# Performance work log

Hardware: AMD Instinct MI355X
Metric: run time of the kernel (lower is better)

Reference implementation:

```python
import jax, jax.numpy as jnp
import numpy as np

BN_EPS = 1e-5


def conv1x1(x, w, b):
    # x: [B,C,H,W], w: [O,C], b: [O] -> [B,O,H,W]
    return jnp.einsum('bchw,oc->bohw', x, w) + b[None, :, None, None]


def setup_inputs() -> dict:
    key = jax.random.key(0)
    ks = jax.random.split(key, 11)
    B, C, H, W = 8, 1024, 64, 32
    hid = 64  # C * rd_ratio (1/16)
    s = 0.02
    return {
        'x': jax.random.normal(ks[0], (B, C, H, W), dtype=jnp.float32),
        'theta_w': jax.random.normal(ks[1], (hid, C), dtype=jnp.float32) * s,
        'theta_b': jax.random.normal(ks[2], (hid,), dtype=jnp.float32) * s,
        'phi_w': jax.random.normal(ks[3], (hid, C), dtype=jnp.float32) * s,
        'phi_b': jax.random.normal(ks[4], (hid,), dtype=jnp.float32) * s,
        'g_w': jax.random.normal(ks[5], (hid, C), dtype=jnp.float32) * s,
        'g_b': jax.random.normal(ks[6], (hid,), dtype=jnp.float32) * s,
        'w_w': jax.random.normal(ks[7], (C, hid), dtype=jnp.float32) * s,
        'w_b': jax.random.normal(ks[8], (C,), dtype=jnp.float32) * s,
        'bn_gamma': jax.random.normal(ks[9], (C,), dtype=jnp.float32) * 0.1 + 1.0,
        'bn_beta': jax.random.normal(ks[10], (C,), dtype=jnp.float32) * 0.1,
    }


def reference(x, theta_w, theta_b, phi_w, phi_b, g_w, g_b, w_w, w_b, bn_gamma, bn_beta):
    B, C, H, W = x.shape
    hid = theta_w.shape[0]
    N = H * W
    theta = conv1x1(x, theta_w, theta_b).reshape(B, hid, N).transpose(0, 2, 1)  # [B,N,d]
    phi = conv1x1(x, phi_w, phi_b).reshape(B, hid, N)                           # [B,d,N]
    g = conv1x1(x, g_w, g_b).reshape(B, hid, N).transpose(0, 2, 1)              # [B,N,d]
    f = jnp.einsum('bnd,bdm->bnm', theta, phi) / N                              # [B,N,N]
    y = jnp.einsum('bnm,bmd->bnd', f, g)                                        # [B,N,d]
    y = y.transpose(0, 2, 1).reshape(B, hid, H, W)
    wy = conv1x1(y, w_w, w_b)                                                   # [B,C,H,W]
    # BatchNorm2d in training mode: batch statistics over (B,H,W), biased variance
    mean = wy.mean(axis=(0, 2, 3), keepdims=True)
    var = wy.var(axis=(0, 2, 3), keepdims=True)
    norm = (wy - mean) * jax.lax.rsqrt(var + BN_EPS)
    out = norm * bn_gamma[None, :, None, None] + bn_beta[None, :, None, None]
    return out + x
```

## Files before the change

### kernel.cpp

```cpp
#include <hip/hip_runtime.h>

#define B_    8
#define C_    1024
#define HID   64
#define N_    2048
#define RTOT  192

typedef __attribute__((ext_vector_type(8))) short   bf16x8;
typedef __attribute__((ext_vector_type(8))) unsigned short ush8;
typedef __attribute__((ext_vector_type(4))) unsigned short ush4;
typedef __attribute__((ext_vector_type(4))) float   f32x4;

#define WSB_WBF   ((size_t)0)
#define WSB_TPG   ((size_t)393216)
#define WSB_THT   ((size_t)6684672)
#define WSB_M     ((size_t)8781824)
#define WSB_G     ((size_t)8912896)
#define WSB_S     ((size_t)9043968)
#define WSB_WMBF  ((size_t)9046016)
#define WSB_SC    ((size_t)10094592)
#define WSB_SH    ((size_t)10098688)
#define WSB_XT    ((size_t)10102784)
#define WSB_P     WSB_XT
#define PSTRIDE   66048
#define POFF_G    32768
#define POFF_S    65536

static __device__ __forceinline__ unsigned short f2bf(float f) {
    union { float f; unsigned u; } v; v.f = f;
    unsigned r = v.u + 0x7fffu + ((v.u >> 16) & 1u);
    return (unsigned short)(r >> 16);
}
static __device__ __forceinline__ float bf2f(unsigned short h) {
    union { unsigned u; float f; } v; v.u = ((unsigned)h) << 16;
    return v.f;
}

static __device__ __forceinline__ void gload16(const unsigned short* g, unsigned short* l) {
    __builtin_amdgcn_global_load_lds(
        (const __attribute__((address_space(1))) unsigned int*)g,
        (__attribute__((address_space(3))) unsigned int*)l, 16, 0, 0);
}

__global__ __launch_bounds__(256) void wcvt(
    const float* __restrict__ tw, const float* __restrict__ pw,
    const float* __restrict__ gw, unsigned short* __restrict__ wbf)
{
    int idx = blockIdx.x * 256 + threadIdx.x;
    int r = idx >> 10, k = idx & 1023;
    float v = (r < 64) ? tw[(size_t)r * 1024 + k]
            : (r < 128) ? pw[(size_t)(r - 64) * 1024 + k]
                        : gw[(size_t)(r - 128) * 1024 + k];
    wbf[idx] = f2bf(v);
}

__global__ __launch_bounds__(256) void xpose(
    const float* __restrict__ x, unsigned short* __restrict__ xT)
{
    const int n0 = blockIdx.x * 64, c0 = blockIdx.y * 64, b = blockIdx.z;
    const int t = threadIdx.x;
    __shared__ unsigned short tile[64][66];

    const float* xb = x + ((size_t)b * C_ + c0) * N_ + n0;
#pragma unroll
    for (int p = 0; p < 2; p++) {
        const int m  = t & 15;
        const int cp = (t >> 4) + 16 * p;
        const int cl = 2 * cp;
        f32x4 v0 = *(const f32x4*)(xb + (size_t)cl * N_ + m * 4);
        f32x4 v1 = *(const f32x4*)(xb + (size_t)(cl + 1) * N_ + m * 4);
#pragma unroll
        for (int r2 = 0; r2 < 4; r2++) {
            unsigned val = (unsigned)f2bf(v0[r2]) | ((unsigned)f2bf(v1[r2]) << 16);
            *(unsigned*)&tile[m * 4 + r2][cl] = val;
        }
    }
    __syncthreads();
    unsigned short* ob = xT + ((size_t)b * N_ + n0) * C_ + c0;
#pragma unroll
    for (int r = 0; r < 2; r++) {
        const int nl   = (t >> 3) + 32 * r;
        const int c8   = (t & 7) * 8;
        uint4 u;
        u.x = *(unsigned*)&tile[nl][c8];
        u.y = *(unsigned*)&tile[nl][c8 + 2];
        u.z = *(unsigned*)&tile[nl][c8 + 4];
        u.w = *(unsigned*)&tile[nl][c8 + 6];
        *(uint4*)(ob + (size_t)nl * C_ + c8) = u;
    }
}

__global__ __launch_bounds__(256, 4) void proj_mfma(
    const unsigned short* __restrict__ xT, const unsigned short* __restrict__ wbf,
    const float* __restrict__ tb, const float* __restrict__ pb,
    const float* __restrict__ gb, unsigned short* __restrict__ tpgbf,
    unsigned short* __restrict__ thT)
{
    const int b = blockIdx.z, rh = blockIdx.y, n0 = blockIdx.x * 64;
    const int t = threadIdx.x, w = t >> 6, L = t & 63;
    const int wn = w & 1, wc = w >> 1;
    const int lr = L & 15, q = L >> 4;

    __shared__ unsigned short Abuf[2][64][64];
    __shared__ unsigned short Bbuf[2][96][64];

    f32x4 acc[2][3] = {};

    auto stage = [&](int cb, int k0) {
#pragma unroll
        for (int i = 0; i < 2; i++) {
            int o = (i * 256 + t) * 16;
            int row = o >> 7, slot = (o >> 4) & 7, ss = slot ^ (row & 7);
            gload16(xT + ((size_t)b * N_ + n0 + row) * C_ + k0 + ss * 8,
                    &Abuf[cb][0][0] + o / 2);
        }
#pragma unroll
        for (int i = 0; i < 3; i++) {
            int o = (i * 256 + t) * 16;
            int row = o >> 7, slot = (o >> 4) & 7, ss = slot ^ (row & 7);
            gload16(wbf + ((size_t)(96 * rh + row)) * 1024 + k0 + ss * 8,
                    &Bbuf[cb][0][0] + o / 2);
        }
    };

    int cur = 0;
    stage(0, 0);
    asm volatile("s_waitcnt vmcnt(0)" ::: "memory");
    __syncthreads();

    const int swz = lr & 7;
    for (int s = 0; s < 16; s++) {
        if (s < 15) stage(cur ^ 1, (s + 1) * 64);
#pragma unroll
        for (int ksub = 0; ksub < 2; ksub++) {
            bf16x8 Af[2], Bf[3];
#pragma unroll
            for (int fa = 0; fa < 2; fa++)
                Af[fa] = *(const bf16x8*)&Abuf[cur][wn * 32 + fa * 16 + lr]
                                               [((ksub * 4 + q) ^ swz) * 8];
#pragma unroll
            for (int j = 0; j < 3; j++)
                Bf[j] = *(const bf16x8*)&Bbuf[cur][wc * 48 + j * 16 + lr]
                                              [((ksub * 4 + q) ^ swz) * 8];
#pragma unroll
            for (int fa = 0; fa < 2; fa++)
#pragma unroll
                for (int j = 0; j < 3; j++)
                    acc[fa][j] = __builtin_amdgcn_mfma_f32_16x16x32_bf16(
                        Af[fa], Bf[j], acc[fa][j], 0, 0, 0);
        }
        asm volatile("s_waitcnt vmcnt(0)" ::: "memory");
        __syncthreads();
        cur ^= 1;
    }

#pragma unroll
    for (int fa = 0; fa < 2; fa++)
#pragma unroll
        for (int j = 0; j < 3; j++) {
            int rcol = 96 * rh + 48 * wc + 16 * j + lr;
            float bias = (rcol < 64) ? tb[rcol]
                       : (rcol < 128) ? pb[rcol - 64] : gb[rcol - 128];
            ush4 o;
#pragma unroll
            for (int rr = 0; rr < 4; rr++) o[rr] = f2bf(acc[fa][j][rr] + bias);
            int nglob = n0 + wn * 32 + fa * 16 + q * 4;
            *(ush4*)(tpgbf + ((size_t)b * RTOT + rcol) * N_ + nglob) = o;
            if (rcol < HID) {
#pragma unroll
                for (int rr = 0; rr < 4; rr++)
                    thT[((size_t)b * N_ + nglob + rr) * HID + rcol] = o[rr];
            }
        }
}

__global__ __launch_bounds__(256) void gram_mfma(
    const unsigned short* __restrict__ tpgbf, float* __restrict__ P)
{
    const int kc = blockIdx.x, p = blockIdx.y, b = blockIdx.z;
    const int t = threadIdx.x, w = t >> 6, L = t & 63;
    const int lr = L & 15, q = L >> 4;
    const unsigned short* base = tpgbf + (size_t)b * RTOT * N_;
    const unsigned short* Arow = base + (p ? 0 : (size_t)64 * N_);
    const unsigned short* Brow = base + (p ? 0 : (size_t)128 * N_);
    const unsigned short* ap = Arow + ((size_t)(16 * w + lr)) * N_ + kc * 256 + q * 8;
    const unsigned short* bp = Brow + ((size_t)lr) * N_ + kc * 256 + q * 8;

    bf16x8 ones;
#pragma unroll
    for (int j = 0; j < 8; j++) ones[j] = (short)0x3F80;

    f32x4 acc[4] = {};
    f32x4 accs = {};
#pragma unroll
    for (int it = 0; it < 8; ++it) {
        const int kn = it * 32;
        bf16x8 a = *(const bf16x8*)(ap + kn);
#pragma unroll
        for (int g = 0; g < 4; g++) {
            bf16x8 bb = *(const bf16x8*)(bp + (size_t)g * 16 * N_ + kn);
            acc[g] = __builtin_amdgcn_mfma_f32_16x16x32_bf16(a, bb, acc[g], 0, 0, 0);
        }
        if (p) accs = __builtin_amdgcn_mfma_f32_16x16x32_bf16(a, ones, accs, 0, 0, 0);
    }
    float* outp = P + (size_t)kc * PSTRIDE + (p ? POFF_G : 0) + b * (HID * HID);
#pragma unroll
    for (int g = 0; g < 4; g++)
#pragma unroll
        for (int r = 0; r < 4; r++) {
            int row = 16 * w + q * 4 + r, col = 16 * g + lr;
            outp[row * HID + col] = acc[g][r];
        }
    if (p && lr == 0) {
#pragma unroll
        for (int r = 0; r < 4; r++)
            P[(size_t)kc * PSTRIDE + POFF_S + b * HID + 16 * w + q * 4 + r] = accs[r];
    }
}

__global__ __launch_bounds__(256) void reduceMGS(
    const float* __restrict__ P, float* __restrict__ out)
{
    int idx = blockIdx.x * 256 + threadIdx.x;
    float s = 0.f;
#pragma unroll
    for (int kc = 0; kc < 8; kc++) s += P[(size_t)kc * PSTRIDE + idx];
    out[idx] = s;
}

__global__ __launch_bounds__(512) void wmstat(
    const float* __restrict__ ww, const float* __restrict__ Mm,
    const float* __restrict__ S, const float* __restrict__ G,
    const float* __restrict__ wb, const float* __restrict__ gamma,
    const float* __restrict__ beta, unsigned short* __restrict__ wmbf,
    float* __restrict__ scale, float* __restrict__ shift2)
{
    const int c = blockIdx.x;
    const int t = threadIdx.x;
    const int b = t >> 6, lane = t & 63;
    const float wbc = wb[c];
    const float* wr = ww + (size_t)c * HID;

    const float* mr = Mm + ((size_t)b * HID + lane) * HID;
    float acc = 0.f;
#pragma unroll
    for (int d = 0; d < HID; d += 4) {
        float4 m4 = *(const float4*)(mr + d);
        acc += wr[d] * m4.x + wr[d + 1] * m4.y + wr[d + 2] * m4.z + wr[d + 3] * m4.w;
    }
    unsigned short us = f2bf(acc * (1.0f / N_));
    wmbf[((size_t)b * C_ + c) * HID + lane] = us;
    float v = bf2f(us);
    float sv = S[b * HID + lane];
    float t1 = v * sv;
    for (int off = 32; off; off >>= 1) t1 += __shfl_down(t1, off);
    t1 = __shfl(t1, 0);

    const f32x4* Gb4 = (const f32x4*)(G + (size_t)b * HID * HID + (size_t)lane * HID);
    float inner = 0.f;
#pragma unroll
    for (int fo = 0; fo < 16; fo++) {
        f32x4 g4 = Gb4[fo];
        inner = fmaf(g4[0], __shfl(v, 4 * fo + 0), inner);
        inner = fmaf(g4[1], __shfl(v, 4 * fo + 1), inner);
        inner = fmaf(g4[2], __shfl(v, 4 * fo + 2), inner);
        inner = fmaf(g4[3], __shfl(v, 4 * fo + 3), inner);
    }
    float qq = v * inner;
    for (int off = 32; off; off >>= 1) qq += __shfl_down(qq, off);
    qq = __shfl(qq, 0);

    __shared__ float red[16];
    if (lane == 0) {
        red[b] = t1;
        red[8 + b] = qq + 2.f * wbc * t1;
    }
    __syncthreads();
    if (t == 0) {
        float asum = 0.f, asq = 0.f;
#pragma unroll
        for (int i = 0; i < 8; i++) { asum += red[i]; asq += red[8 + i]; }
        const float cnt = (float)B_ * (float)N_;
        const float inv = 1.0f / cnt;
        float mean = (asum + cnt * wbc) * inv;
        float e2   = (asq + cnt * wbc * wbc) * inv;
        float var  = e2 - mean * mean;
        float sc   = gamma[c] * rsqrtf(var + 1e-5f);
        scale[c]  = sc;
        shift2[c] = beta[c] - mean * sc + sc * wbc;
    }
}

__global__ __launch_bounds__(256) void finalk_mfma(
    const unsigned short* __restrict__ wmbf, const unsigned short* __restrict__ thT,
    const float* __restrict__ x, const float* __restrict__ scale,
    const float* __restrict__ shift2, float* __restrict__ out)
{
    const int b = blockIdx.z, c0 = blockIdx.y * 64, n0 = blockIdx.x * 64;
    const int t = threadIdx.x, w = t >> 6, L = t & 63;
    const int lr = L & 15, q = L >> 4;

    const unsigned short* ap = thT + ((size_t)b * N_ + n0 + 16 * w + lr) * HID + q * 8;
    const unsigned short* bp = wmbf + ((size_t)b * C_ + c0 + lr) * HID + q * 8;

    float4 xv[4];
    size_t xoff[4];
#pragma unroll
    for (int g = 0; g < 4; g++) {
        xoff[g] = ((size_t)b * C_ + c0 + 16 * g + lr) * N_ + n0 + 16 * w + q * 4;
        xv[g] = *(const float4*)(x + xoff[g]);
    }

    bf16x8 A0 = *(const bf16x8*)(ap);
    bf16x8 A1 = *(const bf16x8*)(ap + 32);
    f32x4 acc[4] = {};
#pragma unroll
    for (int g = 0; g < 4; g++) {
        bf16x8 Bg0 = *(const bf16x8*)(bp + (size_t)g * 16 * HID);
        bf16x8 Bg1 = *(const bf16x8*)(bp + (size_t)g * 16 * HID + 32);
        acc[g] = __builtin_amdgcn_mfma_f32_16x16x32_bf16(A0, Bg0, acc[g], 0, 0, 0);
        acc[g] = __builtin_amdgcn_mfma_f32_16x16x32_bf16(A1, Bg1, acc[g], 0, 0, 0);
    }
#pragma unroll
    for (int g = 0; g < 4; g++) {
        int c = c0 + 16 * g + lr;
        float sc = scale[c], sh = shift2[c];
        float4 o;
        o.x = fmaf(sc, acc[g][0], sh) + xv[g].x;
        o.y = fmaf(sc, acc[g][1], sh) + xv[g].y;
        o.z = fmaf(sc, acc[g][2], sh) + xv[g].z;
        o.w = fmaf(sc, acc[g][3], sh) + xv[g].w;
        *(float4*)(out + xoff[g]) = o;
    }
}

extern "C" void kernel_launch(void* const* d_in, const int* in_sizes, int n_in,
                              void* d_out, int out_size, void* d_ws, size_t ws_size,
                              hipStream_t stream)
{
    const float* x  = (const float*)d_in[0];
    const float* tw = (const float*)d_in[1];
    const float* tb = (const float*)d_in[2];
    const float* pw = (const float*)d_in[3];
    const float* pb = (const float*)d_in[4];
    const float* gw = (const float*)d_in[5];
    const float* gb = (const float*)d_in[6];
    const float* ww = (const float*)d_in[7];
    const float* wb = (const float*)d_in[8];
    const float* gamma = (const float*)d_in[9];
    const float* beta  = (const float*)d_in[10];
    float* out = (float*)d_out;

    char* ws = (char*)d_ws;
    unsigned short* wbf   = (unsigned short*)(ws + WSB_WBF);
    unsigned short* tpgbf = (unsigned short*)(ws + WSB_TPG);
    unsigned short* thT   = (unsigned short*)(ws + WSB_THT);
    float* Mm   = (float*)(ws + WSB_M);
    float* S    = (float*)(ws + WSB_S);
    float* Gg   = (float*)(ws + WSB_G);
    unsigned short* wmbf = (unsigned short*)(ws + WSB_WMBF);
    float* scl  = (float*)(ws + WSB_SC);
    float* shf  = (float*)(ws + WSB_SH);
    unsigned short* xT = (unsigned short*)(ws + WSB_XT);
    float* P    = (float*)(ws + WSB_P);

    wcvt<<<dim3(RTOT * 1024 / 256), 256, 0, stream>>>(tw, pw, gw, wbf);
    xpose<<<dim3(32, 16, B_), 256, 0, stream>>>(x, xT);
    proj_mfma<<<dim3(32, 2, B_), 256, 0, stream>>>(xT, wbf, tb, pb, gb, tpgbf, thT);
    gram_mfma<<<dim3(8, 2, B_), 256, 0, stream>>>(tpgbf, P);
    reduceMGS<<<dim3(258), 256, 0, stream>>>(P, Mm);
    wmstat<<<C_, 512, 0, stream>>>(ww, Mm, S, Gg, wb, gamma, beta, wmbf, scl, shf);
    finalk_mfma<<<dim3(32, 16, B_), 256, 0, stream>>>(wmbf, thT, x, scl, shf, out);
}
```

Measured before the change: 217.5 us.

## Merge weight cast into transpose kernel and drop split-K gram reduction

Fuses the weight bf16 conversion into the transpose kernel as an extra grid slice, and makes the gram kernel accumulate over the full sequence in one block per (pair,batch), writing M, G and S directly. This removes two kernel launches and the partial-sum buffer round trip. In exchange, the gram stage now runs only 16 blocks with a long serial K loop, which sharply lowers its parallelism.

```diff
diff --git a/kernel.cpp b/kernel.cpp
--- a/kernel.cpp
+++ b/kernel.cpp
@@ -21,10 +21,6 @@
 #define WSB_SC    ((size_t)10094592)
 #define WSB_SH    ((size_t)10098688)
 #define WSB_XT    ((size_t)10102784)
-#define WSB_P     WSB_XT
-#define PSTRIDE   66048
-#define POFF_G    32768
-#define POFF_S    65536
 
 static __device__ __forceinline__ unsigned short f2bf(float f) {
     union { float f; unsigned u; } v; v.f = f;
@@ -42,23 +38,28 @@
         (__attribute__((address_space(3))) unsigned int*)l, 16, 0, 0);
 }
 
-__global__ __launch_bounds__(256) void wcvt(
+__global__ __launch_bounds__(256) void prep(
+    const float* __restrict__ x, unsigned short* __restrict__ xT,
     const float* __restrict__ tw, const float* __restrict__ pw,
     const float* __restrict__ gw, unsigned short* __restrict__ wbf)
 {
-    int idx = blockIdx.x * 256 + threadIdx.x;
-    int r = idx >> 10, k = idx & 1023;
-    float v = (r < 64) ? tw[(size_t)r * 1024 + k]
-            : (r < 128) ? pw[(size_t)(r - 64) * 1024 + k]
-                        : gw[(size_t)(r - 128) * 1024 + k];
-    wbf[idx] = f2bf(v);
-}
-
-__global__ __launch_bounds__(256) void xpose(
-    const float* __restrict__ x, unsigned short* __restrict__ xT)
-{
+    const int t = threadIdx.x;
+    if (blockIdx.z == 8) {
+        const int bid = blockIdx.y * 32 + blockIdx.x;
+#pragma unroll
+        for (int rep = 0; rep < 2; rep++) {
+            int idx = bid * 512 + rep * 256 + t;
+            if (idx < RTOT * 1024) {
+                int r = idx >> 10, k = idx & 1023;
+                float v = (r < 64) ? tw[(size_t)r * 1024 + k]
+                        : (r < 128) ? pw[(size_t)(r - 64) * 1024 + k]
+                                    : gw[(size_t)(r - 128) * 1024 + k];
+                wbf[idx] = f2bf(v);
+            }
+        }
+        return;
+    }
     const int n0 = blockIdx.x * 64, c0 = blockIdx.y * 64, b = blockIdx.z;
-    const int t = threadIdx.x;
     __shared__ unsigned short tile[64][66];
 
     const float* xb = x + ((size_t)b * C_ + c0) * N_ + n0;
@@ -175,16 +176,17 @@
 }
 
 __global__ __launch_bounds__(256) void gram_mfma(
-    const unsigned short* __restrict__ tpgbf, float* __restrict__ P)
-{
-    const int kc = blockIdx.x, p = blockIdx.y, b = blockIdx.z;
+    const unsigned short* __restrict__ tpgbf, float* __restrict__ Mm,
+    float* __restrict__ Gg, float* __restrict__ S)
+{
+    const int p = blockIdx.x, b = blockIdx.y;
     const int t = threadIdx.x, w = t >> 6, L = t & 63;
     const int lr = L & 15, q = L >> 4;
     const unsigned short* base = tpgbf + (size_t)b * RTOT * N_;
     const unsigned short* Arow = base + (p ? 0 : (size_t)64 * N_);
     const unsigned short* Brow = base + (p ? 0 : (size_t)128 * N_);
-    const unsigned short* ap = Arow + ((size_t)(16 * w + lr)) * N_ + kc * 256 + q * 8;
-    const unsigned short* bp = Brow + ((size_t)lr) * N_ + kc * 256 + q * 8;
+    const unsigned short* ap = Arow + ((size_t)(16 * w + lr)) * N_ + q * 8;
+    const unsigned short* bp = Brow + ((size_t)lr) * N_ + q * 8;
 
     bf16x8 ones;
 #pragma unroll
@@ -192,8 +194,8 @@
 
     f32x4 acc[4] = {};
     f32x4 accs = {};
-#pragma unroll
-    for (int it = 0; it < 8; ++it) {
+#pragma unroll 4
+    for (int it = 0; it < 64; ++it) {
         const int kn = it * 32;
         bf16x8 a = *(const bf16x8*)(ap + kn);
 #pragma unroll
@@ -203,7 +205,7 @@
         }
         if (p) accs = __builtin_amdgcn_mfma_f32_16x16x32_bf16(a, ones, accs, 0, 0, 0);
     }
-    float* outp = P + (size_t)kc * PSTRIDE + (p ? POFF_G : 0) + b * (HID * HID);
+    float* outp = (p ? Gg : Mm) + (size_t)b * HID * HID;
 #pragma unroll
     for (int g = 0; g < 4; g++)
 #pragma unroll
@@ -214,18 +216,8 @@
     if (p && lr == 0) {
 #pragma unroll
         for (int r = 0; r < 4; r++)
-            P[(size_t)kc * PSTRIDE + POFF_S + b * HID + 16 * w + q * 4 + r] = accs[r];
-    }
-}
-
-__global__ __launch_bounds__(256) void reduceMGS(
-    const float* __restrict__ P, float* __restrict__ out)
-{
-    int idx = blockIdx.x * 256 + threadIdx.x;
-    float s = 0.f;
-#pragma unroll
-    for (int kc = 0; kc < 8; kc++) s += P[(size_t)kc * PSTRIDE + idx];
-    out[idx] = s;
+            S[b * HID + 16 * w + q * 4 + r] = accs[r];
+    }
 }
 
 __global__ __launch_bounds__(512) void wmstat(
@@ -356,19 +348,16 @@
     unsigned short* tpgbf = (unsigned short*)(ws + WSB_TPG);
     unsigned short* thT   = (unsigned short*)(ws + WSB_THT);
     float* Mm   = (float*)(ws + WSB_M);
+    float* Gg   = (float*)(ws + WSB_G);
     float* S    = (float*)(ws + WSB_S);
-    float* Gg   = (float*)(ws + WSB_G);
     unsigned short* wmbf = (unsigned short*)(ws + WSB_WMBF);
     float* scl  = (float*)(ws + WSB_SC);
     float* shf  = (float*)(ws + WSB_SH);
     unsigned short* xT = (unsigned short*)(ws + WSB_XT);
-    float* P    = (float*)(ws + WSB_P);
-
-    wcvt<<<dim3(RTOT * 1024 / 256), 256, 0, stream>>>(tw, pw, gw, wbf);
-    xpose<<<dim3(32, 16, B_), 256, 0, stream>>>(x, xT);
+
+    prep<<<dim3(32, 16, 9), 256, 0, stream>>>(x, xT, tw, pw, gw, wbf);
     proj_mfma<<<dim3(32, 2, B_), 256, 0, stream>>>(xT, wbf, tb, pb, gb, tpgbf, thT);
-    gram_mfma<<<dim3(8, 2, B_), 256, 0, stream>>>(tpgbf, P);
-    reduceMGS<<<dim3(258), 256, 0, stream>>>(P, Mm);
+    gram_mfma<<<dim3(2, B_), 256, 0, stream>>>(tpgbf, Mm, Gg, S);
     wmstat<<<C_, 512, 0, stream>>>(ww, Mm, S, Gg, wb, gamma, beta, wmbf, scl, shf);
     finalk_mfma<<<dim3(32, 16, B_), 256, 0, stream>>>(wmbf, thT, x, scl, shf, out);
 }
```

After: 254.5 us. 1.17x slower.
